# Kernel tuning notes

Measured on AMD Instinct MI355X. Metric: run time of the kernel, lower is better.

Reference implementation:

```python
import jax, jax.numpy as jnp
import numpy as np

B, S, H, STEPS = 4096, 169, 64, 24  # batch, input seq (window 168 + covariate row), hidden, rollout steps


def _lstm(xseq, Wih, Whh, bih, bhh, h0, c0):
    """PyTorch-style single-layer LSTM. xseq: [B,T,D] -> ([B,T,H], hT, cT). Gate order i,f,g,o."""
    xg = jnp.einsum('btd,gd->btg', xseq, Wih) + (bih + bhh)  # precompute input proj [B,T,4H]

    def step(carry, xg_t):
        h, c = carry
        g = xg_t + h @ Whh.T
        i, f, gg, o = jnp.split(g, 4, axis=-1)
        c = jax.nn.sigmoid(f) * c + jax.nn.sigmoid(i) * jnp.tanh(gg)
        h = jax.nn.sigmoid(o) * jnp.tanh(c)
        return (h, c), h

    (hT, cT), hs = jax.lax.scan(step, (h0, c0), jnp.swapaxes(xg, 0, 1))
    return jnp.swapaxes(hs, 0, 1), hT, cT


def reference(x, Wih1, Whh1, bih1, bhh1, Wih2, Whh2, bih2, bhh2, fc1_w, fc1_b, fc2_w, fc2_b):
    win, d = x[:, :-1, :], x[:, -1, :]  # [B,168,1], [B,1]
    z = jnp.zeros((x.shape[0], H), x.dtype)

    def outer(win, _):
        h1s, h1, c1 = _lstm(win, Wih1, Whh1, bih1, bhh1, z, z)
        h1s = jax.nn.relu(h1s)
        # lstm2 is seeded with lstm1's final (h, c) state, as in the torch code
        h2s, _, _ = _lstm(h1s, Wih2, Whh2, bih2, bhh2, h1, c1)
        feat = jnp.concatenate([jax.nn.relu(h2s[:, -1, :]), d], axis=1)  # [B,65]
        out = (feat @ fc1_w.T + fc1_b) @ fc2_w.T + fc2_b  # [B,1] (no relu between fc1/fc2)
        win = jnp.concatenate([win[:, 1:, :], out[:, :, None]], axis=1)  # slide window
        return win, out[:, 0]

    _, outs = jax.lax.scan(outer, win, None, length=STEPS)  # outs: [24,B]
    return jnp.swapaxes(outs, 0, 1)  # [B,24]


def setup_inputs() -> dict:
    key = jax.random.key(0)
    ks = jax.random.split(key, 14)
    bnd = 1.0 / np.sqrt(H)

    def u(k, shape):
        return jax.random.uniform(k, shape, jnp.float32, -bnd, bnd)

    return {
        'x': jax.random.normal(ks[0], (B, S, 1), jnp.float32),
        'Wih1': u(ks[1], (4 * H, 1)),
        'Whh1': u(ks[2], (4 * H, H)),
        'bih1': u(ks[3], (4 * H,)),
        'bhh1': u(ks[4], (4 * H,)),
        'Wih2': u(ks[5], (4 * H, H)),
        'Whh2': u(ks[6], (4 * H, H)),
        'bih2': u(ks[7], (4 * H,)),
        'bhh2': u(ks[8], (4 * H,)),
        'fc1_w': u(ks[9], (64, 65)),
        'fc1_b': u(ks[10], (64,)),
        'fc2_w': u(ks[11], (1, 64)),
        'fc2_b': u(ks[12], (1,)),
    }
```

## Files before the change

### kernel.cpp

```cpp
#include <hip/hip_runtime.h>
#include <stdint.h>

#define NB 16
#define WIN 168
#define NSTEPS 24
#define NBLK (4096/NB)
#define NT 512

typedef __attribute__((ext_vector_type(8))) short bf16x8;
typedef __attribute__((ext_vector_type(4))) float f32x4;
typedef __attribute__((ext_vector_type(2))) float f32x2;

#if __has_builtin(__builtin_amdgcn_rcpf)
#define RCPF(x) __builtin_amdgcn_rcpf(x)
#else
#define RCPF(x) (1.0f / (x))
#endif
#if __has_builtin(__builtin_amdgcn_exp2f)
#define EXP2F(x) __builtin_amdgcn_exp2f(x)
#else
#define EXP2F(x) __expf((x) * 0.6931471805599453f)
#endif

__device__ __forceinline__ float sigm(float x){
  return RCPF(1.0f + EXP2F(x * -1.4426950408889634f));
}
__device__ __forceinline__ float sigtanh(float a, float b){
  float A = EXP2F(a * -1.4426950408889634f);
  float B = EXP2F(fabsf(b) * -2.8853900817779268f);
  float t = (1.0f - B) * RCPF((1.0f + A) * (1.0f + B));
  return __builtin_copysignf(t, b);
}

__device__ __forceinline__ f32x2 exp2v(f32x2 x){ return (f32x2){EXP2F(x.x), EXP2F(x.y)}; }
__device__ __forceinline__ f32x2 rcpv(f32x2 x){ return (f32x2){RCPF(x.x), RCPF(x.y)}; }
__device__ __forceinline__ f32x2 absv(f32x2 x){ return (f32x2){fabsf(x.x), fabsf(x.y)}; }
__device__ __forceinline__ f32x2 csignv(f32x2 t, f32x2 s){
  return (f32x2){__builtin_copysignf(t.x, s.x), __builtin_copysignf(t.y, s.y)};
}
__device__ __forceinline__ f32x2 sigmv(f32x2 x){
  return rcpv(1.0f + exp2v(x * -1.4426950408889634f));
}
__device__ __forceinline__ f32x2 sigtanhv(f32x2 a, f32x2 b){
  f32x2 A = exp2v(a * -1.4426950408889634f);
  f32x2 B = exp2v(absv(b) * -2.8853900817779268f);
  f32x2 t = (1.0f - B) * rcpv((1.0f + A) * (1.0f + B));
  return csignv(t, b);
}

__device__ __forceinline__ uint32_t bf_rn(float f){
  uint32_t u = __builtin_bit_cast(uint32_t, f);
  return (u + 0x7FFFu + ((u >> 16) & 1u)) >> 16;
}
__device__ __forceinline__ float bf_f(uint32_t s){
  return __builtin_bit_cast(float, s << 16);
}
__device__ __forceinline__ void split_t(float f, uint32_t& hi, uint32_t& lo){
  uint32_t u = __builtin_bit_cast(uint32_t, f);
  hi = u >> 16;
  lo = bf_rn(f - bf_f(hi));
}
__device__ __forceinline__ void split_s(float f, short& hi, short& lo){
  uint32_t h = bf_rn(f);
  hi = (short)h;
  lo = (short)bf_rn(f - bf_f(h));
}
__device__ __forceinline__ uint32_t cvtpk2(float a, float b){
  uint32_t r;
  asm("v_cvt_pk_bf16_f32 %0, %1, %2" : "=v"(r) : "v"(a), "v"(b));
  return r;
}
__device__ __forceinline__ float hi_even(uint32_t p){
  return __builtin_bit_cast(float, p << 16);
}
__device__ __forceinline__ float hi_odd(uint32_t p){
  return __builtin_bit_cast(float, p & 0xFFFF0000u);
}
__device__ __forceinline__ f32x4 mfma16(bf16x8 a, bf16x8 b, f32x4 c){
  return __builtin_amdgcn_mfma_f32_16x16x32_bf16(a, b, c, 0, 0, 0);
}

__device__ __forceinline__ void lstm_epi(const f32x4 acc[4], float c[4], float hn[4]){
  #pragma unroll
  for (int p = 0; p < 2; p++){
    const int r0 = 2*p;
    f32x2 gi = {acc[0][r0], acc[0][r0+1]};
    f32x2 gf = {acc[1][r0], acc[1][r0+1]};
    f32x2 gg = {acc[2][r0], acc[2][r0+1]};
    f32x2 go = {acc[3][r0], acc[3][r0+1]};
    f32x2 cc = {c[r0], c[r0+1]};
    f32x2 cn = __builtin_elementwise_fma(sigmv(gf), cc, sigtanhv(gi, gg));
    f32x2 hh = sigtanhv(go, cn);
    c[r0] = cn.x; c[r0+1] = cn.y;
    hn[r0] = hh.x; hn[r0+1] = hh.y;
  }
}

#define FROW 136
#define FBLK 544
#define FB(buf,hl,kt) ((((buf)*2 + (hl))*2 + (kt)) * FBLK)
#define BUF_INTS (2*FBLK)

__device__ __forceinline__ void flag_set(uint32_t* f){
  __threadfence();
  __hip_atomic_store(f, 1u, __ATOMIC_RELEASE, __HIP_MEMORY_SCOPE_AGENT);
}
__device__ __forceinline__ void flag_wait(uint32_t* f){
  while (__hip_atomic_load(f, __ATOMIC_ACQUIRE, __HIP_MEMORY_SCOPE_AGENT) == 0u)
    __builtin_amdgcn_s_sleep(2);
}

__global__ void flags_zero_kernel(uint32_t* flags, int n){
  int i = blockIdx.x*blockDim.x + threadIdx.x;
  if (i < n) flags[i] = 0u;
}

__global__ __launch_bounds__(256, 2) void lstm_pipe_kernel(
  const float* __restrict__ x,    const float* __restrict__ Wih1, const float* __restrict__ Whh1,
  const float* __restrict__ bih1, const float* __restrict__ bhh1,
  const float* __restrict__ Wih2, const float* __restrict__ Whh2,
  const float* __restrict__ bih2, const float* __restrict__ bhh2,
  const float* __restrict__ fc1w, const float* __restrict__ fc1b,
  const float* __restrict__ fc2w, const float* __restrict__ fc2b,
  float* __restrict__ out, short* __restrict__ hist,
  short* __restrict__ hoff, float* __restrict__ cg, uint32_t* __restrict__ flags)
{
  __shared__ __align__(16) short aS[2*2*2*FBLK];
  __shared__ __align__(16) short bS[2*2*2*FBLK];
  __shared__ float win_s[WIN][NB];
  __shared__ float Hlast[NB][68];
  __shared__ float fc1w_s[64*68];
  __shared__ float dval_s[NB];

  const int b   = blockIdx.x >> 1;
  const bool isA = ((blockIdx.x & 1) == 0);
  const int tid = threadIdx.x;
  const int wv  = tid >> 6;
  const int ln  = tid & 63;
  const int q   = ln >> 4;
  const int n   = ln & 15;
  const int bg0 = b * NB;
  const int u0  = 16*wv + 4*q;
  const int kt_  = u0 >> 5;
  const int q2_  = (u0 >> 3) & 3;
  const int jj0_ = u0 & 7;
  const int rdo  = q*FROW + n*8;
  const int wro  = q2_*FROW + n*8 + jj0_;
  const int gwo  = kt_*512 + q2_*128 + n*8 + jj0_;
  const int ro   = q*128 + n*8;

  short* __restrict__ hoffb = hoff + (size_t)b * (4*FBLK);
  float* __restrict__ cgb   = cg + (size_t)b * 1024;
  uint32_t* flagA  = flags + (size_t)b * 64;
  uint32_t* flagFC = flags + (size_t)b * 64 + 32;
  short* hb = nullptr;

  if (isA){
    for (int i = tid; i < WIN*NB; i += 256){ int t = i >> 4, bb = i & 15; win_s[t][bb] = x[(bg0 + bb)*169 + t]; }

    bf16x8 A1hi[4][2], A1lo[4][2], Ain1[4];
    f32x4 b1c[4];
    #pragma unroll
    for (int e = 0; e < 4; e++){
      const int ja = 64*e + 16*wv + n;
      #pragma unroll
      for (int kt = 0; kt < 2; kt++){
        const float* pw = Whh1 + ja*64 + kt*32 + q*8;
        #pragma unroll
        for (int jj = 0; jj < 8; jj++){ short h,l; split_s(pw[jj], h, l); A1hi[e][kt][jj] = h; A1lo[e][kt][jj] = l; }
      }
      bf16x8 ain = {0,0,0,0,0,0,0,0};
      if (q == 0){ short wh, wl; split_s(Wih1[ja], wh, wl); ain[0] = wh; ain[1] = wh; ain[2] = wl; }
      Ain1[e] = ain;
      const int jc = 64*e + u0;
      #pragma unroll
      for (int r = 0; r < 4; r++) b1c[e][r] = bih1[jc+r] + bhh1[jc+r];
    }
    float c1[4];

    auto lstm1 = [&](int rb, int wb, float xv, int t, bool first, bool fin){
      f32x4 acc[4];
      bf16x8 bin = {0,0,0,0,0,0,0,0};
      { uint32_t xp = cvtpk2(xv, xv);
        float rx = xv - hi_even(xp);
        uint32_t xq = cvtpk2(rx, rx);
        if (q == 0){ bin[0] = (short)xp; bin[1] = (short)xq; bin[2] = (short)xp; } }
      if (first){
        #pragma unroll
        for (int e = 0; e < 4; e++) acc[e] = mfma16(Ain1[e], bin, b1c[e]);
      } else {
        bf16x8 Bh0 = *(const bf16x8*)&aS[FB(rb,0,0)+rdo];
        bf16x8 Bl0 = *(const bf16x8*)&aS[FB(rb,1,0)+rdo];
        bf16x8 Bh1 = *(const bf16x8*)&aS[FB(rb,0,1)+rdo];
        bf16x8 Bl1 = *(const bf16x8*)&aS[FB(rb,1,1)+rdo];
        #pragma unroll
        for (int e = 0; e < 4; e++){
          f32x4 a = b1c[e];
          a = mfma16(A1hi[e][0], Bh0, a);
          a = mfma16(A1hi[e][0], Bl0, a);
          a = mfma16(A1lo[e][0], Bh0, a);
          a = mfma16(A1hi[e][1], Bh1, a);
          a = mfma16(A1hi[e][1], Bl1, a);
          a = mfma16(A1lo[e][1], Bh1, a);
          a = mfma16(Ain1[e], bin, a);
          acc[e] = a;
        }
      }
      float hn[4];
      lstm_epi(acc, c1, hn);
      uint32_t p01 = cvtpk2(hn[0], hn[1]);
      uint32_t p23 = cvtpk2(hn[2], hn[3]);
      f32x2 r01 = (f32x2){hn[0], hn[1]} - (f32x2){hi_even(p01), hi_odd(p01)};
      f32x2 r23 = (f32x2){hn[2], hn[3]} - (f32x2){hi_even(p23), hi_odd(p23)};
      uint32_t q01 = cvtpk2(r01.x, r01.y);
      uint32_t q23 = cvtpk2(r23.x, r23.y);
      *(uint2*)&aS[FB(wb,0,kt_)+wro] = make_uint2(p01, p23);
      *(uint2*)&aS[FB(wb,1,kt_)+wro] = make_uint2(q01, q23);
      uint32_t m01 = (hn[0] > 0.0f ? 0x0000FFFFu : 0u) | (hn[1] > 0.0f ? 0xFFFF0000u : 0u);
      uint32_t m23 = (hn[2] > 0.0f ? 0x0000FFFFu : 0u) | (hn[3] > 0.0f ? 0xFFFF0000u : 0u);
      short* Hp = hb + (size_t)t * 2048;
      *(uint2*)&Hp[gwo]        = make_uint2(p01 & m01, p23 & m23);
      *(uint2*)&Hp[1024 + gwo] = make_uint2(q01 & m01, q23 & m23);
      if (fin){
        *(uint2*)&hoffb[FB(0,0,kt_)+wro] = make_uint2(p01, p23);
        *(uint2*)&hoffb[FB(0,1,kt_)+wro] = make_uint2(q01, q23);
      }
    };

    auto getx = [&](int sg, int t)->float{
      int s = sg + t;
      if (s < WIN) return win_s[s][n];
      return out[(bg0 + n)*24 + (s - WIN)];
    };

    for (int sg = 0; sg < NSTEPS; sg++){
      hb = hist + ((size_t)((sg & 1)*NBLK + b)) * WIN * 2048;
      #pragma unroll
      for (int r = 0; r < 4; r++) c1[r] = 0.0f;
      __syncthreads();
      lstm1(0, 1, getx(sg, 0), 0, true, false);
      for (int t = 1; t < WIN-1; t += 2){
        __syncthreads();
        lstm1(1, 0, getx(sg, t), t, false, false);
        __syncthreads();
        lstm1(0, 1, getx(sg, t+1), t+1, false, false);
      }
      if (sg >= 1){
        if (tid == 0) flag_wait(&flagFC[sg-1]);
        __syncthreads();
        __threadfence();
      }
      __syncthreads();
      lstm1(1, 0, getx(sg, WIN-1), WIN-1, false, true);
      #pragma unroll
      for (int r = 0; r < 4; r++) cgb[(u0 + r)*16 + n] = c1[r];
      __syncthreads();
      if (tid == 0) flag_set(&flagA[sg]);
    }

  } else {
    for (int i = tid; i < 64*65; i += 256){ int j = i / 65, k = i % 65; fc1w_s[j*68 + k] = fc1w[i]; }
    if (tid < NB) dval_s[tid] = x[(bg0 + tid)*169 + 168];

    const float fc1b_r = fc1b[ln];
    const float fc2w_r = fc2w[ln];
    const float fc2b_r = fc2b[0];

    bf16x8 A2hi[4][4], A2lo[4][4];
    f32x4 b2c[4];
    #pragma unroll
    for (int e = 0; e < 4; e++){
      const int ja = 64*e + 16*wv + n;
      #pragma unroll
      for (int kt = 0; kt < 4; kt++){
        const float* pw = (kt < 2 ? (Wih2 + ja*64 + kt*32) : (Whh2 + ja*64 + (kt-2)*32)) + q*8;
        #pragma unroll
        for (int jj = 0; jj < 8; jj++){ short h,l; split_s(pw[jj], h, l); A2hi[e][kt][jj] = h; A2lo[e][kt][jj] = l; }
      }
      const int jc = 64*e + u0;
      #pragma unroll
      for (int r = 0; r < 4; r++) b2c[e][r] = bih2[jc+r] + bhh2[jc+r];
    }
    float c2[4];
    bf16x8 ch0, cl0, ch1, cl1, nh0, nl0, nh1, nl1;

    auto loadc = [&](int t){
      const short* Hp = hb + (size_t)t * 2048;
      ch0 = *(const bf16x8*)&Hp[ro];
      cl0 = *(const bf16x8*)&Hp[1024 + ro];
      ch1 = *(const bf16x8*)&Hp[512 + ro];
      cl1 = *(const bf16x8*)&Hp[1536 + ro];
    };
    auto loadn = [&](int t){
      const short* Hp = hb + (size_t)t * 2048;
      nh0 = *(const bf16x8*)&Hp[ro];
      nl0 = *(const bf16x8*)&Hp[1024 + ro];
      nh1 = *(const bf16x8*)&Hp[512 + ro];
      nl1 = *(const bf16x8*)&Hp[1536 + ro];
    };
    auto shift = [&](){ ch0 = nh0; cl0 = nl0; ch1 = nh1; cl1 = nl1; };

    auto lstm2 = [&](const short* Sr, int rb, short* Sw, int wb, bool last){
      bf16x8 L2h0 = *(const bf16x8*)&Sr[FB(rb,0,0)+rdo];
      bf16x8 L2l0 = *(const bf16x8*)&Sr[FB(rb,1,0)+rdo];
      bf16x8 L2h1 = *(const bf16x8*)&Sr[FB(rb,0,1)+rdo];
      bf16x8 L2l1 = *(const bf16x8*)&Sr[FB(rb,1,1)+rdo];
      f32x4 acc[4];
      #pragma unroll
      for (int e = 0; e < 4; e++){
        f32x4 a = b2c[e];
        a = mfma16(A2hi[e][0], ch0, a);
        a = mfma16(A2hi[e][0], cl0, a);
        a = mfma16(A2lo[e][0], ch0, a);
        a = mfma16(A2hi[e][1], ch1, a);
        a = mfma16(A2hi[e][1], cl1, a);
        a = mfma16(A2lo[e][1], ch1, a);
        a = mfma16(A2hi[e][2], L2h0, a);
        a = mfma16(A2hi[e][2], L2l0, a);
        a = mfma16(A2lo[e][2], L2h0, a);
        a = mfma16(A2hi[e][3], L2h1, a);
        a = mfma16(A2hi[e][3], L2l1, a);
        a = mfma16(A2lo[e][3], L2h1, a);
        acc[e] = a;
      }
      float hn[4];
      lstm_epi(acc, c2, hn);
      if (!last){
        uint32_t p01 = cvtpk2(hn[0], hn[1]);
        uint32_t p23 = cvtpk2(hn[2], hn[3]);
        f32x2 r01 = (f32x2){hn[0], hn[1]} - (f32x2){hi_even(p01), hi_odd(p01)};
        f32x2 r23 = (f32x2){hn[2], hn[3]} - (f32x2){hi_even(p23), hi_odd(p23)};
        *(uint2*)&Sw[FB(wb,0,kt_)+wro] = make_uint2(p01, p23);
        *(uint2*)&Sw[FB(wb,1,kt_)+wro] = make_uint2(cvtpk2(r01.x, r01.y), cvtpk2(r23.x, r23.y));
      } else {
        #pragma unroll
        for (int r = 0; r < 4; r++) Hlast[n][u0 + r] = fmaxf(hn[r], 0.0f);
      }
    };

    auto fc_head = [&](int s){
      float o4[4];
      #pragma unroll
      for (int bi = 0; bi < 4; bi++){
        const int b4 = 4*wv + bi;
        float a1 = fc1b_r;
        #pragma unroll
        for (int k4 = 0; k4 < 16; k4++){
          const float* wp = &fc1w_s[ln*68 + k4*4];
          const float* hp = &Hlast[b4][k4*4];
          a1 += wp[0]*hp[0] + wp[1]*hp[1] + wp[2]*hp[2] + wp[3]*hp[3];
        }
        a1 += dval_s[b4] * fc1w_s[ln*68 + 64];
        float v = a1 * fc2w_r;
        #pragma unroll
        for (int off = 32; off > 0; off >>= 1) v += __shfl_xor(v, off);
        o4[bi] = v + fc2b_r;
      }
      if (ln == 0){
        #pragma unroll
        for (int bi = 0; bi < 4; bi++){
          const int b4 = 4*wv + bi;
          out[(bg0 + b4)*24 + s] = o4[bi];
        }
      }
    };

    for (int sg = 0; sg < NSTEPS; sg++){
      if (tid == 0) flag_wait(&flagA[sg]);
      __syncthreads();
      __threadfence();
      hb = hist + ((size_t)((sg & 1)*NBLK + b)) * WIN * 2048;
      #pragma unroll
      for (int r = 0; r < 4; r++) c2[r] = cgb[(u0 + r)*16 + n];
      loadc(0);
      loadn(1);
      lstm2(hoffb, 0, bS, 1, false);
      shift();
      for (int t = 1; t < WIN-1; t += 2){
        __syncthreads();
        loadn(t + 1);
        lstm2(bS, 1, bS, 0, false);
        shift();
        __syncthreads();
        loadn(t + 2);
        lstm2(bS, 0, bS, 1, false);
        shift();
      }
      __syncthreads();
      lstm2(bS, 1, bS, 0, true);
      __syncthreads();
      fc_head(sg);
      __syncthreads();
      if (tid == 0) flag_set(&flagFC[sg]);
    }
  }
}

__global__ __launch_bounds__(NT, 2) void lstm_fused_kernel(
  const float* __restrict__ x,    const float* __restrict__ Wih1, const float* __restrict__ Whh1,
  const float* __restrict__ bih1, const float* __restrict__ bhh1,
  const float* __restrict__ Wih2, const float* __restrict__ Whh2,
  const float* __restrict__ bih2, const float* __restrict__ bhh2,
  const float* __restrict__ fc1w, const float* __restrict__ fc1b,
  const float* __restrict__ fc2w, const float* __restrict__ fc2b,
  float* __restrict__ out, short* __restrict__ hist)
{
  __shared__ __align__(16) short aS[2*2*2*FBLK];
  __shared__ __align__(16) short bS[2*2*2*FBLK];
  __shared__ float cS[64][16];
  __shared__ float win_s[WIN][NB];
  __shared__ float Hlast[NB][68];
  __shared__ float fc1w_s[64*68];
  __shared__ float dval_s[NB];

  const int tid = threadIdx.x;
  const int wv8 = tid >> 6;
  const int wv  = wv8 & 3;
  const bool isA = (wv8 < 4);
  const int ln  = tid & 63;
  const int q   = ln >> 4;
  const int n   = ln & 15;
  const int bg0 = blockIdx.x * NB;
  const int u0  = 16*wv + 4*q;
  const int kt_  = u0 >> 5;
  const int q2_  = (u0 >> 3) & 3;
  const int jj0_ = u0 & 7;
  const int rdo  = q*FROW + n*8;
  const int wro  = q2_*FROW + n*8 + jj0_;
  const int gwo  = kt_*512 + q2_*128 + n*8 + jj0_;
  const int ro   = q*128 + n*8;
  short* __restrict__ hblk = hist + (size_t)blockIdx.x * WIN * 2048;

  for (int i = tid; i < WIN*NB; i += NT){ int t = i >> 4, b = i & 15; win_s[t][b] = x[(bg0 + b)*169 + t]; }
  for (int i = tid; i < 64*65; i += NT){ int j = i / 65, k = i % 65; fc1w_s[j*68 + k] = fc1w[i]; }
  if (tid < NB) dval_s[tid] = x[(bg0 + tid)*169 + 168];

  const float fc1b_r = fc1b[ln];
  const float fc2w_r = fc2w[ln];
  const float fc2b_r = fc2b[0];

  auto fc_head = [&](int s){
    float o2[2];
    #pragma unroll
    for (int bi = 0; bi < 2; bi++){
      const int b = 2*wv8 + bi;
      float a1 = fc1b_r;
      #pragma unroll
      for (int k4 = 0; k4 < 16; k4++){
        const float* wp = &fc1w_s[ln*68 + k4*4];
        const float* hp = &Hlast[b][k4*4];
        a1 += wp[0]*hp[0] + wp[1]*hp[1] + wp[2]*hp[2] + wp[3]*hp[3];
      }
      a1 += dval_s[b] * fc1w_s[ln*68 + 64];
      float v = a1 * fc2w_r;
      #pragma unroll
      for (int off = 32; off > 0; off >>= 1) v += __shfl_xor(v, off);
      o2[bi] = v + fc2b_r;
    }
    if (ln == 0){
      #pragma unroll
      for (int bi = 0; bi < 2; bi++){
        const int b = 2*wv8 + bi;
        out[(bg0 + b)*24 + s] = o2[bi];
        win_s[s % WIN][b] = o2[bi];
      }
    }
  };

  if (isA){
    bf16x8 A1hi[4][2], A1lo[4][2], Ain1[4];
    f32x4 b1c[4];
    #pragma unroll
    for (int e = 0; e < 4; e++){
      const int ja = 64*e + 16*wv + n;
      #pragma unroll
      for (int kt = 0; kt < 2; kt++){
        const float* pw = Whh1 + ja*64 + kt*32 + q*8;
        #pragma unroll
        for (int jj = 0; jj < 8; jj++){ short h,l; split_s(pw[jj], h, l); A1hi[e][kt][jj] = h; A1lo[e][kt][jj] = l; }
      }
      bf16x8 ain = {0,0,0,0,0,0,0,0};
      if (q == 0){ short wh, wl; split_s(Wih1[ja], wh, wl); ain[0] = wh; ain[1] = wh; ain[2] = wl; }
      Ain1[e] = ain;
      const int jc = 64*e + u0;
      #pragma unroll
      for (int r = 0; r < 4; r++) b1c[e][r] = bih1[jc+r] + bhh1[jc+r];
    }
    float c1[4];

    auto lstm1 = [&](int rb, int wb, int slot, int t, bool first){
      f32x4 acc[4];
      bf16x8 bin = {0,0,0,0,0,0,0,0};
      { float xv = win_s[slot][n];
        uint32_t xp = cvtpk2(xv, xv);
        float rx = xv - hi_even(xp);
        uint32_t xq = cvtpk2(rx, rx);
        if (q == 0){ bin[0] = (short)xp; bin[1] = (short)xq; bin[2] = (short)xp; } }
      if (first){
        #pragma unroll
        for (int e = 0; e < 4; e++) acc[e] = mfma16(Ain1[e], bin, b1c[e]);
      } else {
        bf16x8 Bh0 = *(const bf16x8*)&aS[FB(rb,0,0)+rdo];
        bf16x8 Bl0 = *(const bf16x8*)&aS[FB(rb,1,0)+rdo];
        bf16x8 Bh1 = *(const bf16x8*)&aS[FB(rb,0,1)+rdo];
        bf16x8 Bl1 = *(const bf16x8*)&aS[FB(rb,1,1)+rdo];
        #pragma unroll
        for (int e = 0; e < 4; e++){
          f32x4 a = b1c[e];
          a = mfma16(A1hi[e][0], Bh0, a);
          a = mfma16(A1hi[e][0], Bl0, a);
          a = mfma16(A1lo[e][0], Bh0, a);
          a = mfma16(A1hi[e][1], Bh1, a);
          a = mfma16(A1hi[e][1], Bl1, a);
          a = mfma16(A1lo[e][1], Bh1, a);
          a = mfma16(Ain1[e], bin, a);
          acc[e] = a;
        }
      }
      float hn[4];
      lstm_epi(acc, c1, hn);
      uint32_t p01 = cvtpk2(hn[0], hn[1]);
      uint32_t p23 = cvtpk2(hn[2], hn[3]);
      f32x2 r01 = (f32x2){hn[0], hn[1]} - (f32x2){hi_even(p01), hi_odd(p01)};
      f32x2 r23 = (f32x2){hn[2], hn[3]} - (f32x2){hi_even(p23), hi_odd(p23)};
      uint32_t q01 = cvtpk2(r01.x, r01.y);
      uint32_t q23 = cvtpk2(r23.x, r23.y);
      *(uint2*)&aS[FB(wb,0,kt_)+wro] = make_uint2(p01, p23);
      *(uint2*)&aS[FB(wb,1,kt_)+wro] = make_uint2(q01, q23);
      uint32_t m01 = (hn[0] > 0.0f ? 0x0000FFFFu : 0u) | (hn[1] > 0.0f ? 0xFFFF0000u : 0u);
      uint32_t m23 = (hn[2] > 0.0f ? 0x0000FFFFu : 0u) | (hn[3] > 0.0f ? 0xFFFF0000u : 0u);
      short* Hp = hblk + (size_t)t * 2048;
      *(uint2*)&Hp[gwo]        = make_uint2(p01 & m01, p23 & m23);
      *(uint2*)&Hp[1024 + gwo] = make_uint2(q01 & m01, q23 & m23);
    };

    #pragma unroll
    for (int r = 0; r < 4; r++) c1[r] = 0.0f;
    __syncthreads();
    lstm1(0, 1, 0, 0, true);
    for (int t = 1; t < WIN-1; t += 2){
      __syncthreads();
      lstm1(1, 0, t, t, false);
      __syncthreads();
      lstm1(0, 1, t+1, t+1, false);
    }
    __syncthreads();
    lstm1(1, 0, WIN-1, WIN-1, false);
    #pragma unroll
    for (int r = 0; r < 4; r++) cS[u0 + r][n] = c1[r];

    for (int sg = 1; sg < NSTEPS; sg++){
      #pragma unroll
      for (int r = 0; r < 4; r++) c1[r] = 0.0f;
      int slot = sg;
      __syncthreads();
      lstm1(0, 1, slot, 0, true);
      slot++;
      for (int t = 1; t < WIN-1; t += 2){
        __syncthreads();
        lstm1(1, 0, slot, t, false);
        slot++; if (slot == WIN) slot = 0;
        __syncthreads();
        lstm1(0, 1, slot, t+1, false);
        slot++; if (slot == WIN) slot = 0;
      }
      __syncthreads();
      __syncthreads();
      fc_head(sg - 1);
      __syncthreads();
      lstm1(1, 0, slot, WIN-1, false);
      #pragma unroll
      for (int r = 0; r < 4; r++) cS[u0 + r][n] = c1[r];
    }

    for (int i = 0; i < WIN + 1; i++) __syncthreads();
    fc_head(NSTEPS - 1);

  } else {
    bf16x8 A2hi[4][4], A2lo[4][4];
    f32x4 b2c[4];
    #pragma unroll
    for (int e = 0; e < 4; e++){
      const int ja = 64*e + 16*wv + n;
      #pragma unroll
      for (int kt = 0; kt < 4; kt++){
        const float* pw = (kt < 2 ? (Wih2 + ja*64 + kt*32) : (Whh2 + ja*64 + (kt-2)*32)) + q*8;
        #pragma unroll
        for (int jj = 0; jj < 8; jj++){ short h,l; split_s(pw[jj], h, l); A2hi[e][kt][jj] = h; A2lo[e][kt][jj] = l; }
      }
      const int jc = 64*e + u0;
      #pragma unroll
      for (int r = 0; r < 4; r++) b2c[e][r] = bih2[jc+r] + bhh2[jc+r];
    }
    float c2[4];
    bf16x8 ch0, cl0, ch1, cl1, nh0, nl0, nh1, nl1;

    auto loadc = [&](int t){
      const short* Hp = hblk + (size_t)t * 2048;
      ch0 = *(const bf16x8*)&Hp[ro];
      cl0 = *(const bf16x8*)&Hp[1024 + ro];
      ch1 = *(const bf16x8*)&Hp[512 + ro];
      cl1 = *(const bf16x8*)&Hp[1536 + ro];
    };
    auto loadn = [&](int t){
      const short* Hp = hblk + (size_t)t * 2048;
      nh0 = *(const bf16x8*)&Hp[ro];
      nl0 = *(const bf16x8*)&Hp[1024 + ro];
      nh1 = *(const bf16x8*)&Hp[512 + ro];
      nl1 = *(const bf16x8*)&Hp[1536 + ro];
    };
    auto shift = [&](){ ch0 = nh0; cl0 = nl0; ch1 = nh1; cl1 = nl1; };

    auto lstm2 = [&](const short* Sr, int rb, short* Sw, int wb, bool last){
      bf16x8 L2h0 = *(const bf16x8*)&Sr[FB(rb,0,0)+rdo];
      bf16x8 L2l0 = *(const bf16x8*)&Sr[FB(rb,1,0)+rdo];
      bf16x8 L2h1 = *(const bf16x8*)&Sr[FB(rb,0,1)+rdo];
      bf16x8 L2l1 = *(const bf16x8*)&Sr[FB(rb,1,1)+rdo];
      f32x4 acc[4];
      #pragma unroll
      for (int e = 0; e < 4; e++){
        f32x4 a = b2c[e];
        a = mfma16(A2hi[e][0], ch0, a);
        a = mfma16(A2hi[e][0], cl0, a);
        a = mfma16(A2lo[e][0], ch0, a);
        a = mfma16(A2hi[e][1], ch1, a);
        a = mfma16(A2hi[e][1], cl1, a);
        a = mfma16(A2lo[e][1], ch1, a);
        a = mfma16(A2hi[e][2], L2h0, a);
        a = mfma16(A2hi[e][2], L2l0, a);
        a = mfma16(A2lo[e][2], L2h0, a);
        a = mfma16(A2hi[e][3], L2h1, a);
        a = mfma16(A2hi[e][3], L2l1, a);
        a = mfma16(A2lo[e][3], L2h1, a);
        acc[e] = a;
      }
      float hn[4];
      lstm_epi(acc, c2, hn);
      if (!last){
        uint32_t p01 = cvtpk2(hn[0], hn[1]);
        uint32_t p23 = cvtpk2(hn[2], hn[3]);
        f32x2 r01 = (f32x2){hn[0], hn[1]} - (f32x2){hi_even(p01), hi_odd(p01)};
        f32x2 r23 = (f32x2){hn[2], hn[3]} - (f32x2){hi_even(p23), hi_odd(p23)};
        *(uint2*)&Sw[FB(wb,0,kt_)+wro] = make_uint2(p01, p23);
        *(uint2*)&Sw[FB(wb,1,kt_)+wro] = make_uint2(cvtpk2(r01.x, r01.y), cvtpk2(r23.x, r23.y));
      } else {
        #pragma unroll
        for (int r = 0; r < 4; r++) Hlast[n][u0 + r] = fmaxf(hn[r], 0.0f);
      }
    };

    for (int i = 0; i < WIN; i++) __syncthreads();

    for (int sg = 1; sg < NSTEPS; sg++){
      loadc(0);
      loadn(1);
      __syncthreads();
      #pragma unroll
      for (int r = 0; r < 4; r++) c2[r] = cS[u0 + r][n];
      lstm2(aS, 0, bS, 1, false);
      shift();
      for (int t = 1; t < WIN-1; t += 2){
        __syncthreads();
        loadn(t + 1);
        lstm2(bS, 1, bS, 0, false);
        shift();
        __syncthreads();
        loadn(t + 2);
        lstm2(bS, 0, bS, 1, false);
        shift();
      }
      __syncthreads();
      lstm2(bS, 1, bS, 0, true);
      __syncthreads();
      fc_head(sg - 1);
      __syncthreads();
    }

    {
      loadc(0);
      loadn(1);
      __syncthreads();
      #pragma unroll
      for (int r = 0; r < 4; r++) c2[r] = cS[u0 + r][n];
      lstm2(aS, 0, bS, 1, false);
      shift();
      for (int t = 1; t < WIN-1; t += 2){
        __syncthreads();
        loadn(t + 1);
        lstm2(bS, 1, bS, 0, false);
        shift();
        __syncthreads();
        loadn(t + 2);
        lstm2(bS, 0, bS, 1, false);
        shift();
      }
      __syncthreads();
      lstm2(bS, 1, bS, 0, true);
      __syncthreads();
      fc_head(NSTEPS - 1);
    }
  }
}

__global__ __launch_bounds__(256, 1) void lstm_fallback_kernel(
  const float* __restrict__ x,    const float* __restrict__ Wih1, const float* __restrict__ Whh1,
  const float* __restrict__ bih1, const float* __restrict__ bhh1,
  const float* __restrict__ Wih2, const float* __restrict__ Whh2,
  const float* __restrict__ bih2, const float* __restrict__ bhh2,
  const float* __restrict__ fc1w, const float* __restrict__ fc1b,
  const float* __restrict__ fc2w, const float* __restrict__ fc2b,
  float* __restrict__ out)
{
  __shared__ __align__(16) short aS[2*2*2*FBLK];
  __shared__ __align__(16) short r1f[2*2*2*FBLK];
  __shared__ __align__(16) short rlf[2*2*2*FBLK];
  __shared__ float win_s[WIN][NB];
  __shared__ float Hlast[NB][68];
  __shared__ float fc1w_s[64*68];
  __shared__ float dval_s[NB];

  const int tid = threadIdx.x;
  const int wv  = tid >> 6;
  const int ln  = tid & 63;
  const int q   = ln >> 4;
  const int n   = ln & 15;
  const int bg0 = blockIdx.x * NB;
  const int u0  = 16*wv + 4*q;
  const int kt_  = u0 >> 5;
  const int q2_  = (u0 >> 3) & 3;
  const int jj0_ = u0 & 7;
  const int rdo  = q*FROW + n*8;
  const int wro  = q2_*FROW + n*8 + jj0_;

  for (int i = tid; i < WIN*NB; i += 256){ int t = i >> 4, b = i & 15; win_s[t][b] = x[(bg0 + b)*169 + t]; }
  for (int i = tid; i < 64*65; i += 256){ int j = i / 65, k = i % 65; fc1w_s[j*68 + k] = fc1w[i]; }
  if (tid < NB) dval_s[tid] = x[(bg0 + tid)*169 + 168];

  const float fc1b_r = fc1b[ln];
  const float fc2w_r = fc2w[ln];
  const float fc2b_r = fc2b[0];

  bf16x8 A1hi[4][2], A1lo[4][2], Ain1[4];
  bf16x8 A2hi[4][4], A2lo[4][4];
  f32x4 b1c[4], b2c[4];
  #pragma unroll
  for (int e = 0; e < 4; e++){
    const int ja = 64*e + 16*wv + n;
    #pragma unroll
    for (int kt = 0; kt < 2; kt++){
      const float* pw = Whh1 + ja*64 + kt*32 + q*8;
      #pragma unroll
      for (int jj = 0; jj < 8; jj++){ short h,l; split_s(pw[jj], h, l); A1hi[e][kt][jj] = h; A1lo[e][kt][jj] = l; }
    }
    #pragma unroll
    for (int kt = 0; kt < 4; kt++){
      const float* pw = (kt < 2 ? (Wih2 + ja*64 + kt*32) : (Whh2 + ja*64 + (kt-2)*32)) + q*8;
      #pragma unroll
      for (int jj = 0; jj < 8; jj++){ short h,l; split_s(pw[jj], h, l); A2hi[e][kt][jj] = h; A2lo[e][kt][jj] = l; }
    }
    bf16x8 ain = {0,0,0,0,0,0,0,0};
    if (q == 0){ short wh, wl; split_s(Wih1[ja], wh, wl); ain[0] = wh; ain[1] = wh; ain[2] = wl; }
    Ain1[e] = ain;
    const int jc = 64*e + u0;
    #pragma unroll
    for (int r = 0; r < 4; r++){
      b1c[e][r] = bih1[jc+r] + bhh1[jc+r];
      b2c[e][r] = bih2[jc+r] + bhh2[jc+r];
    }
  }

  float c1[4], c2[4], c1r[4];

  auto lstm1_step = [&](short* S, float* cst, int rb, int wb, int slot, bool relu_out){
    bf16x8 Bh0 = *(const bf16x8*)&S[FB(rb,0,0)+rdo];
    bf16x8 Bl0 = *(const bf16x8*)&S[FB(rb,1,0)+rdo];
    bf16x8 Bh1 = *(const bf16x8*)&S[FB(rb,0,1)+rdo];
    bf16x8 Bl1 = *(const bf16x8*)&S[FB(rb,1,1)+rdo];
    bf16x8 bin = {0,0,0,0,0,0,0,0};
    { float xv = win_s[slot][n]; uint32_t xh, xl; split_t(xv, xh, xl);
      if (q == 0){ bin[0] = (short)xh; bin[1] = (short)xl; bin[2] = (short)xh; } }
    f32x4 acc[4];
    #pragma unroll
    for (int e = 0; e < 4; e++){
      f32x4 a = b1c[e];
      a = mfma16(A1hi[e][0], Bh0, a);
      a = mfma16(A1hi[e][0], Bl0, a);
      a = mfma16(A1lo[e][0], Bh0, a);
      a = mfma16(A1hi[e][1], Bh1, a);
      a = mfma16(A1hi[e][1], Bl1, a);
      a = mfma16(A1lo[e][1], Bh1, a);
      a = mfma16(Ain1[e], bin, a);
      acc[e] = a;
    }
    float hn[4];
    #pragma unroll
    for (int r = 0; r < 4; r++){
      float cn = __builtin_fmaf(sigm(acc[1][r]), cst[r], sigtanh(acc[0][r], acc[2][r]));
      cst[r] = cn;
      hn[r] = sigtanh(acc[3][r], cn);
    }
    uint32_t ph[4], pl[4];
    #pragma unroll
    for (int r = 0; r < 4; r++) split_t(hn[r], ph[r], pl[r]);
    *(uint2*)&S[FB(wb,0,kt_)+wro] = make_uint2(ph[0] | (ph[1]<<16), ph[2] | (ph[3]<<16));
    *(uint2*)&S[FB(wb,1,kt_)+wro] = make_uint2(pl[0] | (pl[1]<<16), pl[2] | (pl[3]<<16));
    if (relu_out){
      uint32_t sh[4], sl[4];
      #pragma unroll
      for (int r = 0; r < 4; r++){ bool pos = hn[r] > 0.0f; sh[r] = pos ? ph[r] : 0u; sl[r] = pos ? pl[r] : 0u; }
      *(uint2*)&rlf[FB(rb,0,kt_)+wro] = make_uint2(sh[0] | (sh[1]<<16), sh[2] | (sh[3]<<16));
      *(uint2*)&rlf[FB(rb,1,kt_)+wro] = make_uint2(sl[0] | (sl[1]<<16), sl[2] | (sl[3]<<16));
    }
  };

  auto lstm2_core = [&](bf16x8 L1h0, bf16x8 L1l0, bf16x8 L1h1, bf16x8 L1l1,
                        int rbuf, int wbuf, bool last){
    bf16x8 L2h0 = *(const bf16x8*)&aS[FB(rbuf,0,0)+rdo];
    bf16x8 L2l0 = *(const bf16x8*)&aS[FB(rbuf,1,0)+rdo];
    bf16x8 L2h1 = *(const bf16x8*)&aS[FB(rbuf,0,1)+rdo];
    bf16x8 L2l1 = *(const bf16x8*)&aS[FB(rbuf,1,1)+rdo];
    f32x4 acc[4];
    #pragma unroll
    for (int e = 0; e < 4; e++){
      f32x4 a = b2c[e];
      a = mfma16(A2hi[e][0], L1h0, a);
      a = mfma16(A2hi[e][0], L1l0, a);
      a = mfma16(A2lo[e][0], L1h0, a);
      a = mfma16(A2hi[e][1], L1h1, a);
      a = mfma16(A2hi[e][1], L1l1, a);
      a = mfma16(A2lo[e][1], L1h1, a);
      a = mfma16(A2hi[e][2], L2h0, a);
      a = mfma16(A2hi[e][2], L2l0, a);
      a = mfma16(A2lo[e][2], L2h0, a);
      a = mfma16(A2hi[e][3], L2h1, a);
      a = mfma16(A2hi[e][3], L2l1, a);
      a = mfma16(A2lo[e][3], L2h1, a);
      acc[e] = a;
    }
    float hn[4];
    #pragma unroll
    for (int r = 0; r < 4; r++){
      float cn = __builtin_fmaf(sigm(acc[1][r]), c2[r], sigtanh(acc[0][r], acc[2][r]));
      c2[r] = cn;
      hn[r] = sigtanh(acc[3][r], cn);
    }
    if (!last){
      uint32_t ph[4], pl[4];
      #pragma unroll
      for (int r = 0; r < 4; r++) split_t(hn[r], ph[r], pl[r]);
      *(uint2*)&aS[FB(wbuf,0,kt_)+wro] = make_uint2(ph[0] | (ph[1]<<16), ph[2] | (ph[3]<<16));
      *(uint2*)&aS[FB(wbuf,1,kt_)+wro] = make_uint2(pl[0] | (pl[1]<<16), pl[2] | (pl[3]<<16));
    } else {
      #pragma unroll
      for (int r = 0; r < 4; r++) Hlast[n][u0 + r] = fmaxf(hn[r], 0.0f);
    }
  };

  for (int s = 0; s < NSTEPS; s++){
    { int* p = (int*)&aS[0];
      for (int i = tid; i < BUF_INTS; i += 256) p[i] = 0; }
    #pragma unroll
    for (int r = 0; r < 4; r++) c1[r] = 0.0f;
    int slot = s;
    for (int t = 0; t < WIN; t++){
      __syncthreads();
      lstm1_step(aS, c1, t & 1, (t & 1) ^ 1, slot, false);
      slot++; if (slot == WIN) slot = 0;
    }
    #pragma unroll
    for (int r = 0; r < 4; r++){ c2[r] = c1[r]; c1r[r] = 0.0f; }
    { int* p = (int*)&r1f[0];
      for (int i = tid; i < BUF_INTS; i += 256) p[i] = 0; }
    slot = s;
    __syncthreads();
    lstm1_step(r1f, c1r, 0, 1, slot, true);
    slot++;
    for (int i = 1; i < WIN; i++){
      __syncthreads();
      const int rb = i & 1, wb = rb ^ 1;
      lstm1_step(r1f, c1r, rb, wb, slot, true);
      bf16x8 L1h0 = *(const bf16x8*)&rlf[FB(wb,0,0)+rdo];
      bf16x8 L1l0 = *(const bf16x8*)&rlf[FB(wb,1,0)+rdo];
      bf16x8 L1h1 = *(const bf16x8*)&rlf[FB(wb,0,1)+rdo];
      bf16x8 L1l1 = *(const bf16x8*)&rlf[FB(wb,1,1)+rdo];
      lstm2_core(L1h0, L1l0, L1h1, L1l1, wb, rb, false);
      slot++; if (slot == WIN) slot = 0;
    }
    __syncthreads();
    {
      const int rb = (WIN - 1) & 1;
      bf16x8 L1h0 = *(const bf16x8*)&rlf[FB(rb,0,0)+rdo];
      bf16x8 L1l0 = *(const bf16x8*)&rlf[FB(rb,1,0)+rdo];
      bf16x8 L1h1 = *(const bf16x8*)&rlf[FB(rb,0,1)+rdo];
      bf16x8 L1l1 = *(const bf16x8*)&rlf[FB(rb,1,1)+rdo];
      lstm2_core(L1h0, L1l0, L1h1, L1l1, rb, 0, true);
    }
    __syncthreads();
    {
      float o4[4];
      #pragma unroll
      for (int bi = 0; bi < 4; bi++){
        const int b = 4*wv + bi;
        float a1 = fc1b_r;
        #pragma unroll
        for (int k4 = 0; k4 < 16; k4++){
          const float* wp = &fc1w_s[ln*68 + k4*4];
          const float* hp = &Hlast[b][k4*4];
          a1 += wp[0]*hp[0] + wp[1]*hp[1] + wp[2]*hp[2] + wp[3]*hp[3];
        }
        a1 += dval_s[b] * fc1w_s[ln*68 + 64];
        float v = a1 * fc2w_r;
        #pragma unroll
        for (int off = 32; off > 0; off >>= 1) v += __shfl_xor(v, off);
        o4[bi] = v + fc2b_r;
      }
      if (ln == 0){
        #pragma unroll
        for (int bi = 0; bi < 4; bi++){
          const int b = 4*wv + bi;
          out[(bg0 + b)*24 + s] = o4[bi];
          win_s[s % WIN][b] = o4[bi];
        }
      }
    }
  }
}

extern "C" void kernel_launch(void* const* d_in, const int* in_sizes, int n_in,
                              void* d_out, int out_size, void* d_ws, size_t ws_size,
                              hipStream_t stream) {
  (void)in_sizes; (void)n_in; (void)out_size;
  const size_t histB = (size_t)2 * NBLK * WIN * 2048 * sizeof(short);
  const size_t hoffB = (size_t)NBLK * 4 * FBLK * sizeof(short);
  const size_t cgB   = (size_t)NBLK * 1024 * sizeof(float);
  const size_t flagB = (size_t)NBLK * 64 * sizeof(uint32_t);
  const size_t needP = histB + hoffB + cgB + flagB;
  const size_t needF = (size_t)NBLK * WIN * 2048 * sizeof(short);

  if (ws_size >= needP){
    short* hist = (short*)d_ws;
    short* hoff = (short*)((char*)d_ws + histB);
    float* cg   = (float*)((char*)d_ws + histB + hoffB);
    uint32_t* flags = (uint32_t*)((char*)d_ws + histB + hoffB + cgB);
    const int nflags = NBLK * 64;
    flags_zero_kernel<<<dim3((nflags + 255)/256), dim3(256), 0, stream>>>(flags, nflags);
    lstm_pipe_kernel<<<dim3(2*NBLK), dim3(256), 0, stream>>>(
        (const float*)d_in[0], (const float*)d_in[1], (const float*)d_in[2],
        (const float*)d_in[3], (const float*)d_in[4], (const float*)d_in[5],
        (const float*)d_in[6], (const float*)d_in[7], (const float*)d_in[8],
        (const float*)d_in[9], (const float*)d_in[10], (const float*)d_in[11],
        (const float*)d_in[12], (float*)d_out, hist, hoff, cg, flags);
  } else if (ws_size >= needF){
    lstm_fused_kernel<<<dim3(NBLK), dim3(NT), 0, stream>>>(
        (const float*)d_in[0], (const float*)d_in[1], (const float*)d_in[2],
        (const float*)d_in[3], (const float*)d_in[4], (const float*)d_in[5],
        (const float*)d_in[6], (const float*)d_in[7], (const float*)d_in[8],
        (const float*)d_in[9], (const float*)d_in[10], (const float*)d_in[11],
        (const float*)d_in[12], (float*)d_out, (short*)d_ws);
  } else {
    lstm_fallback_kernel<<<dim3(NBLK), dim3(256), 0, stream>>>(
        (const float*)d_in[0], (const float*)d_in[1], (const float*)d_in[2],
        (const float*)d_in[3], (const float*)d_in[4], (const float*)d_in[5],
        (const float*)d_in[6], (const float*)d_in[7], (const float*)d_in[8],
        (const float*)d_in[9], (const float*)d_in[10], (const float*)d_in[11],
        (const float*)d_in[12], (float*)d_out);
  }
}
```

Before: 4.762 ms.

## Single-buffer hidden history with chunked producer-consumer flags between LSTM blocks

Replaces the double-buffered per-step hidden-state history with a single buffer per batch group. Reuse is guarded by four chunk flags: the consumer (LSTM2) block marks progress through the history, and the producer (LSTM1) block waits on the matching chunk before overwriting it. Block assignment changes from interleaved even/odd to first half producers and second half consumers, and the chunk flags use relaxed atomics. The intent is to halve the history footprint so it stays in cache, at the cost of extra cross-block waits. Relaxed ordering on the chunk flags may be a correctness risk for the write-after-read reuse.

```diff
diff --git a/kernel.cpp b/kernel.cpp
--- a/kernel.cpp
+++ b/kernel.cpp
@@ -101,12 +101,19 @@
 #define FB(buf,hl,kt) ((((buf)*2 + (hl))*2 + (kt)) * FBLK)
 #define BUF_INTS (2*FBLK)
 
-__device__ __forceinline__ void flag_set(uint32_t* f){
+__device__ __forceinline__ void flag_set_rel(uint32_t* f){
   __threadfence();
   __hip_atomic_store(f, 1u, __ATOMIC_RELEASE, __HIP_MEMORY_SCOPE_AGENT);
 }
-__device__ __forceinline__ void flag_wait(uint32_t* f){
+__device__ __forceinline__ void flag_set_rlx(uint32_t* f){
+  __hip_atomic_store(f, 1u, __ATOMIC_RELAXED, __HIP_MEMORY_SCOPE_AGENT);
+}
+__device__ __forceinline__ void flag_wait_acq(uint32_t* f){
   while (__hip_atomic_load(f, __ATOMIC_ACQUIRE, __HIP_MEMORY_SCOPE_AGENT) == 0u)
+    __builtin_amdgcn_s_sleep(2);
+}
+__device__ __forceinline__ void flag_wait_rlx(uint32_t* f){
+  while (__hip_atomic_load(f, __ATOMIC_RELAXED, __HIP_MEMORY_SCOPE_AGENT) == 0u)
     __builtin_amdgcn_s_sleep(2);
 }
 
@@ -132,8 +139,8 @@
   __shared__ float fc1w_s[64*68];
   __shared__ float dval_s[NB];
 
-  const int b   = blockIdx.x >> 1;
-  const bool isA = ((blockIdx.x & 1) == 0);
+  const bool isA = (blockIdx.x < NBLK);
+  const int b   = blockIdx.x & (NBLK - 1);
   const int tid = threadIdx.x;
   const int wv  = tid >> 6;
   const int ln  = tid & 63;
@@ -149,11 +156,13 @@
   const int gwo  = kt_*512 + q2_*128 + n*8 + jj0_;
   const int ro   = q*128 + n*8;
 
+  short* __restrict__ hblk  = hist + (size_t)b * WIN * 2048;
   short* __restrict__ hoffb = hoff + (size_t)b * (4*FBLK);
   float* __restrict__ cgb   = cg + (size_t)b * 1024;
-  uint32_t* flagA  = flags + (size_t)b * 64;
-  uint32_t* flagFC = flags + (size_t)b * 64 + 32;
-  short* hb = nullptr;
+  uint32_t* fl    = flags + (size_t)b * 256;
+  uint32_t* flagA  = fl;
+  uint32_t* flagFC = fl + 32;
+  uint32_t* flagsB = fl + 64;
 
   if (isA){
     for (int i = tid; i < WIN*NB; i += 256){ int t = i >> 4, bb = i & 15; win_s[t][bb] = x[(bg0 + bb)*169 + t]; }
@@ -218,7 +227,7 @@
       *(uint2*)&aS[FB(wb,1,kt_)+wro] = make_uint2(q01, q23);
       uint32_t m01 = (hn[0] > 0.0f ? 0x0000FFFFu : 0u) | (hn[1] > 0.0f ? 0xFFFF0000u : 0u);
       uint32_t m23 = (hn[2] > 0.0f ? 0x0000FFFFu : 0u) | (hn[3] > 0.0f ? 0xFFFF0000u : 0u);
-      short* Hp = hb + (size_t)t * 2048;
+      short* Hp = hblk + (size_t)t * 2048;
       *(uint2*)&Hp[gwo]        = make_uint2(p01 & m01, p23 & m23);
       *(uint2*)&Hp[1024 + gwo] = make_uint2(q01 & m01, q23 & m23);
       if (fin){
@@ -229,33 +238,36 @@
 
     auto getx = [&](int sg, int t)->float{
       int s = sg + t;
-      if (s < WIN) return win_s[s][n];
-      return out[(bg0 + n)*24 + (s - WIN)];
+      return (s < WIN) ? win_s[s][n] : out[(bg0 + n)*24 + (s - WIN)];
     };
 
     for (int sg = 0; sg < NSTEPS; sg++){
-      hb = hist + ((size_t)((sg & 1)*NBLK + b)) * WIN * 2048;
+      if (sg >= 1){ if (tid == 0) flag_wait_rlx(&flagsB[4*(sg-1) + 0]); }
+      __syncthreads();
       #pragma unroll
       for (int r = 0; r < 4; r++) c1[r] = 0.0f;
-      __syncthreads();
       lstm1(0, 1, getx(sg, 0), 0, true, false);
       for (int t = 1; t < WIN-1; t += 2){
         __syncthreads();
         lstm1(1, 0, getx(sg, t), t, false, false);
         __syncthreads();
+        if (sg >= 1 && (t == 41 || t == 83 || t == 125)){
+          if (tid == 0) flag_wait_rlx(&flagsB[4*(sg-1) + (t+1)/42]);
+          __syncthreads();
+        }
         lstm1(0, 1, getx(sg, t+1), t+1, false, false);
       }
+      __syncthreads();
       if (sg >= 1){
-        if (tid == 0) flag_wait(&flagFC[sg-1]);
+        if (tid == 0) flag_wait_acq(&flagFC[sg-1]);
         __syncthreads();
         __threadfence();
       }
-      __syncthreads();
       lstm1(1, 0, getx(sg, WIN-1), WIN-1, false, true);
       #pragma unroll
       for (int r = 0; r < 4; r++) cgb[(u0 + r)*16 + n] = c1[r];
       __syncthreads();
-      if (tid == 0) flag_set(&flagA[sg]);
+      if (tid == 0) flag_set_rel(&flagA[sg]);
     }
 
   } else {
@@ -285,14 +297,14 @@
     bf16x8 ch0, cl0, ch1, cl1, nh0, nl0, nh1, nl1;
 
     auto loadc = [&](int t){
-      const short* Hp = hb + (size_t)t * 2048;
+      const short* Hp = hblk + (size_t)t * 2048;
       ch0 = *(const bf16x8*)&Hp[ro];
       cl0 = *(const bf16x8*)&Hp[1024 + ro];
       ch1 = *(const bf16x8*)&Hp[512 + ro];
       cl1 = *(const bf16x8*)&Hp[1536 + ro];
     };
     auto loadn = [&](int t){
-      const short* Hp = hb + (size_t)t * 2048;
+      const short* Hp = hblk + (size_t)t * 2048;
       nh0 = *(const bf16x8*)&Hp[ro];
       nl0 = *(const bf16x8*)&Hp[1024 + ro];
       nh1 = *(const bf16x8*)&Hp[512 + ro];
@@ -366,10 +378,9 @@
     };
 
     for (int sg = 0; sg < NSTEPS; sg++){
-      if (tid == 0) flag_wait(&flagA[sg]);
+      if (tid == 0) flag_wait_acq(&flagA[sg]);
       __syncthreads();
       __threadfence();
-      hb = hist + ((size_t)((sg & 1)*NBLK + b)) * WIN * 2048;
       #pragma unroll
       for (int r = 0; r < 4; r++) c2[r] = cgb[(u0 + r)*16 + n];
       loadc(0);
@@ -385,13 +396,17 @@
         loadn(t + 2);
         lstm2(bS, 0, bS, 1, false);
         shift();
-      }
-      __syncthreads();
+        if (t == 41 || t == 83 || t == 125){
+          if (tid == 0) flag_set_rlx(&flagsB[4*sg + (t-41)/42]);
+        }
+      }
+      __syncthreads();
+      if (tid == 0) flag_set_rlx(&flagsB[4*sg + 3]);
       lstm2(bS, 1, bS, 0, true);
       __syncthreads();
       fc_head(sg);
       __syncthreads();
-      if (tid == 0) flag_set(&flagFC[sg]);
+      if (tid == 0) flag_set_rel(&flagFC[sg]);
     }
   }
 }
@@ -930,19 +945,19 @@
                               void* d_out, int out_size, void* d_ws, size_t ws_size,
                               hipStream_t stream) {
   (void)in_sizes; (void)n_in; (void)out_size;
-  const size_t histB = (size_t)2 * NBLK * WIN * 2048 * sizeof(short);
+  const size_t histB = (size_t)NBLK * WIN * 2048 * sizeof(short);
   const size_t hoffB = (size_t)NBLK * 4 * FBLK * sizeof(short);
   const size_t cgB   = (size_t)NBLK * 1024 * sizeof(float);
-  const size_t flagB = (size_t)NBLK * 64 * sizeof(uint32_t);
+  const size_t flagB = (size_t)NBLK * 256 * sizeof(uint32_t);
   const size_t needP = histB + hoffB + cgB + flagB;
-  const size_t needF = (size_t)NBLK * WIN * 2048 * sizeof(short);
+  const size_t needF = histB;
 
   if (ws_size >= needP){
     short* hist = (short*)d_ws;
     short* hoff = (short*)((char*)d_ws + histB);
     float* cg   = (float*)((char*)d_ws + histB + hoffB);
     uint32_t* flags = (uint32_t*)((char*)d_ws + histB + hoffB + cgB);
-    const int nflags = NBLK * 64;
+    const int nflags = NBLK * 256;
     flags_zero_kernel<<<dim3((nflags + 255)/256), dim3(256), 0, stream>>>(flags, nflags);
     lstm_pipe_kernel<<<dim3(2*NBLK), dim3(256), 0, stream>>>(
         (const float*)d_in[0], (const float*)d_in[1], (const float*)d_in[2],
```

Result: slower. 8.499 ms (+78.5%).
